# Kernel optimization log

Measured on AMD Instinct MI355X. Metric: run time of the kernel, lower is better.

Reference implementation:

```python
import jax, jax.numpy as jnp
import numpy as np

N = 4096
NFEAT = 256
NHID1 = 64
NHID2 = 32
NCLASS = 8
NHEADS = 4
NADJ = 2
ALPHA = 0.2  # leaky relu slope
NEG = -9e15


def setup_inputs() -> dict:
    key = jax.random.key(0)
    ks = jax.random.split(key, 14)
    x = jax.random.normal(ks[0], (N, NFEAT), jnp.float32)
    adj = (jax.random.uniform(ks[1], (NADJ, N, N)) < 0.01).astype(jnp.float32)
    adj = jnp.maximum(adj, jnp.eye(N, dtype=jnp.float32)[None])
    s = 0.05
    W1 = jax.random.normal(ks[2], (NADJ, NHEADS, NFEAT, NHID1), jnp.float32) * s
    a1 = jax.random.normal(ks[3], (NADJ, NHEADS, 2, NHID1), jnp.float32) * s
    W2 = jax.random.normal(ks[4], (NADJ, NHEADS, NHID1, NHID2), jnp.float32) * s
    a2 = jax.random.normal(ks[5], (NADJ, NHEADS, 2, NHID2), jnp.float32) * s
    Wi1 = jax.random.normal(ks[6], (NHID1 * NHEADS, NHID1), jnp.float32) * s
    bi1 = jnp.zeros((NHID1,), jnp.float32)
    Wi2 = jax.random.normal(ks[7], (NHID2 * NHEADS, NCLASS), jnp.float32) * s
    bi2 = jnp.zeros((NCLASS,), jnp.float32)
    Wf = jax.random.normal(ks[8], (NCLASS * NADJ, NCLASS), jnp.float32) * s
    bf = jnp.zeros((NCLASS,), jnp.float32)
    return {"x": x, "adj": adj, "W1": W1, "a1": a1, "W2": W2, "a2": a2,
            "Wi1": Wi1, "bi1": bi1, "Wi2": Wi2, "bi2": bi2, "Wf": Wf, "bf": bf}


def gat_multihead(x, adj_i, W, a):
    # x: [n, f]; adj_i: [n, n]; W: [h, f, o]; a: [h, 2, o]
    Wh = jnp.einsum('nf,hfo->hno', x, W)                 # [h, n, o]
    f_src = jnp.einsum('hno,ho->hn', Wh, a[:, 0])        # [h, n]
    f_dst = jnp.einsum('hno,ho->hn', Wh, a[:, 1])        # [h, n]
    e = jax.nn.leaky_relu(f_src[:, :, None] + f_dst[:, None, :], ALPHA)
    e = jnp.where(adj_i[None] > 0, e, NEG)               # masked scores [h, n, n]
    att = jax.nn.softmax(e, axis=-1)
    h = jnp.einsum('hnm,hmo->hno', att, Wh)              # aggregate
    h = jax.nn.elu(h)                                     # concat=True -> elu
    n = x.shape[0]
    return jnp.transpose(h, (1, 0, 2)).reshape(n, -1)     # [n, h*o]


def reference(x, adj, W1, a1, W2, a2, Wi1, bi1, Wi2, bi2, Wf, bf):
    outs = []
    for i in range(NADJ):  # small fixed loop over adjacency graphs
        xi = gat_multihead(x, adj[i], W1[i], a1[i])
        xi = jax.nn.elu(xi @ Wi1 + bi1)
        xi = gat_multihead(xi, adj[i], W2[i], a2[i])
        xi = jax.nn.elu(xi @ Wi2 + bi2)
        outs.append(xi)
    out = jnp.concatenate(outs, axis=1) @ Wf + bf         # [n, nclass]
    l1_loss = jnp.mean(jnp.abs(Wf))
    return jax.nn.log_softmax(out, axis=1), l1_loss
```

## Files before the change

### kernel.cpp

```cpp
#include <hip/hip_runtime.h>
#include <hip/hip_bf16.h>

#define NN 4096
#define NFEAT 256
#define NHID1 64
#define NHID2 32
#define NCLASS 8
#define NHEADS 4
#define NADJ 2
#define CAP 128

__device__ __forceinline__ unsigned short f2bf(float v) {
  unsigned int x = __float_as_uint(v);
  return (unsigned short)((x + 0x7fffu + ((x >> 16) & 1u)) >> 16);
}

template <int KDIM, int NDIM, int RPTY>
__device__ __forceinline__ void gemm_body(
    const float* __restrict__ A, const float* __restrict__ B,
    unsigned short* __restrict__ C, const float* __restrict__ ag,
    float* __restrict__ fsrc, float* __restrict__ fdst, const int row0b,
    float* __restrict__ sA, float* __restrict__ sB) {
  constexpr int KT = 32;
  constexpr int TX = NDIM / 4;
  constexpr int TY = 256 / TX;
  constexpr int BR = TY * RPTY;
  constexpr int LDA = BR + 4;
  constexpr int LDB = NDIM + 4;
  const int tid = threadIdx.x;
  const int tx = tid % TX, ty = tid / TX;
  const int c0 = tx * 4;
  float acc[RPTY][4];
#pragma unroll
  for (int i = 0; i < RPTY; ++i)
#pragma unroll
    for (int j = 0; j < 4; ++j) acc[i][j] = 0.f;

  for (int kt = 0; kt < KDIM; kt += KT) {
    __syncthreads();
    for (int i = tid; i < BR * (KT / 4); i += 256) {
      const int r = i / (KT / 4), e = i % (KT / 4);
      const float4 v = *(const float4*)(A + (size_t)(row0b + r) * KDIM + kt + e * 4);
      sA[(e * 4 + 0) * LDA + r] = v.x;
      sA[(e * 4 + 1) * LDA + r] = v.y;
      sA[(e * 4 + 2) * LDA + r] = v.z;
      sA[(e * 4 + 3) * LDA + r] = v.w;
    }
    for (int i = tid; i < KT * (NDIM / 4); i += 256) {
      const int k = i / (NDIM / 4), cc = i % (NDIM / 4);
      *(float4*)&sB[k * LDB + cc * 4] = *(const float4*)(B + (size_t)(kt + k) * NDIM + cc * 4);
    }
    __syncthreads();
#pragma unroll
    for (int k = 0; k < KT; ++k) {
      const float4 t = *(const float4*)&sA[k * LDA + ty * 4];
      const float a4[4] = {t.x, t.y, t.z, t.w};
      const float4 bv = *(const float4*)&sB[k * LDB + c0];
      const float b4[4] = {bv.x, bv.y, bv.z, bv.w};
#pragma unroll
      for (int i = 0; i < RPTY; ++i)
#pragma unroll
        for (int j = 0; j < 4; ++j) acc[i][j] += a4[i] * b4[j];
    }
  }
#pragma unroll
  for (int i = 0; i < RPTY; ++i) {
    const int row = row0b + ty * RPTY + i;
    ushort4 o;
    o.x = f2bf(acc[i][0]); o.y = f2bf(acc[i][1]);
    o.z = f2bf(acc[i][2]); o.w = f2bf(acc[i][3]);
    *(ushort4*)(C + (size_t)row * NDIM + c0) = o;
  }
  float aS[4], aD[4];
#pragma unroll
  for (int j = 0; j < 4; ++j) { aS[j] = ag[c0 + j]; aD[j] = ag[NDIM + c0 + j]; }
#pragma unroll
  for (int i = 0; i < RPTY; ++i) {
    float s = 0.f, d = 0.f;
#pragma unroll
    for (int j = 0; j < 4; ++j) { s += acc[i][j] * aS[j]; d += acc[i][j] * aD[j]; }
#pragma unroll
    for (int off = TX / 2; off; off >>= 1) {
      s += __shfl_xor(s, off);
      d += __shfl_xor(d, off);
    }
    if (tx == 0) {
      const int row = row0b + ty * RPTY + i;
      fsrc[row] = s;
      fdst[row] = d;
    }
  }
}

__global__ __launch_bounds__(256) void k1_gemm_edges(
    const float* __restrict__ x, const float* __restrict__ W1,
    const float* __restrict__ a1, unsigned short* __restrict__ Wh1,
    float* __restrict__ fs1, float* __restrict__ fd1,
    const float* __restrict__ adj, int* __restrict__ eidx,
    int* __restrict__ ecnt) {
  __shared__ float sA[32 * (64 + 4)];
  __shared__ float sB[32 * (64 + 4)];
  constexpr int NB_GEMM = (NN / 64) * NHEADS * NADJ;
  if (blockIdx.x < NB_GEMM) {
    int b = blockIdx.x;
    const int tile = b % (NN / 64); b /= (NN / 64);
    const int h = b % NHEADS;
    const int g = b / NHEADS;
    const int gh = g * NHEADS + h;
    gemm_body<NFEAT, NHID1, 4>(
        x, W1 + (size_t)gh * NFEAT * NHID1, Wh1 + (size_t)gh * NN * NHID1,
        a1 + (size_t)gh * 2 * NHID1, fs1 + (size_t)gh * NN,
        fd1 + (size_t)gh * NN, tile * 64, sA, sB);
  } else {
    const int wave = threadIdx.x >> 6;
    const int lane = threadIdx.x & 63;
    const int r = (blockIdx.x - NB_GEMM) * 4 + wave;
    const float4* row = (const float4*)(adj + (size_t)r * NN);
    int* out = eidx + (size_t)r * CAP;
    int base = 0;
    for (int c = 0; c < NN; c += 256) {
      const float4 v = row[(c >> 2) + lane];
      const int j0 = c + lane * 4;
      const float vt[4] = {v.x, v.y, v.z, v.w};
#pragma unroll
      for (int t = 0; t < 4; ++t) {
        const bool hit = vt[t] > 0.f;
        const unsigned long long m = __ballot(hit);
        if (hit) {
          const int pos = base + __popcll(m & ((1ull << lane) - 1ull));
          if (pos < CAP) out[pos] = j0 + t;
        }
        base += __popcll(m);
      }
    }
    if (lane == 0) ecnt[r] = base < CAP ? base : CAP;
  }
}

#define GATB(ACC, JJ, OO)                                                      \
  {                                                                            \
    const float w_ = wgt[wave][JJ];                                            \
    const uint4 v_ = *(const uint4*)(WhH + (size_t)midx[wave][JJ] * OO + c8);  \
    ACC[0] += w_ * __uint_as_float(v_.x << 16);                                \
    ACC[1] += w_ * __uint_as_float(v_.x & 0xffff0000u);                        \
    ACC[2] += w_ * __uint_as_float(v_.y << 16);                                \
    ACC[3] += w_ * __uint_as_float(v_.y & 0xffff0000u);                        \
    ACC[4] += w_ * __uint_as_float(v_.z << 16);                                \
    ACC[5] += w_ * __uint_as_float(v_.z & 0xffff0000u);                        \
    ACC[6] += w_ * __uint_as_float(v_.w << 16);                                \
    ACC[7] += w_ * __uint_as_float(v_.w & 0xffff0000u);                        \
  }

__global__ __launch_bounds__(256) void aggregate1(
    const unsigned short* __restrict__ Wh, const float* __restrict__ fsrc,
    const float* __restrict__ fdst, const int* __restrict__ eidx,
    const int* __restrict__ ecnt, float* __restrict__ Hout) {
  constexpr int O = NHID1;
  constexpr int CPL = O / 8;
  constexpr int EPW = 64 / CPL;
  __shared__ float wgt[4][CAP];
  __shared__ int midx[4][CAP];
  const int wave = threadIdx.x >> 6;
  const int lane = threadIdx.x & 63;
  const int n = blockIdx.x * 4 + wave;
  const int h = blockIdx.y, g = blockIdx.z;
  const int gh = g * NHEADS + h;
  const int cnt = ecnt[(size_t)g * NN + n];
  const int* ei = eidx + (size_t)(g * NN + n) * CAP;
  const float fs = fsrc[(size_t)gh * NN + n];
  const float* fd = fdst + (size_t)gh * NN;
  float mx = -3.4e38f;
  for (int j = lane; j < cnt; j += 64) {
    const int m = ei[j];
    float e = fs + fd[m];
    e = e > 0.f ? e : 0.2f * e;
    midx[wave][j] = m;
    wgt[wave][j] = e;
    mx = fmaxf(mx, e);
  }
  for (int off = 32; off; off >>= 1) mx = fmaxf(mx, __shfl_xor(mx, off));
  float sm = 0.f;
  for (int j = lane; j < cnt; j += 64) {
    const float w = __expf(wgt[wave][j] - mx);
    wgt[wave][j] = w;
    sm += w;
  }
  for (int off = 32; off; off >>= 1) sm += __shfl_xor(sm, off);
  const unsigned short* WhH = Wh + (size_t)gh * NN * O;
  const int sub = lane / CPL;
  const int c8 = (lane % CPL) * 8;
  float A0[8] = {0, 0, 0, 0, 0, 0, 0, 0};
  float A1[8] = {0, 0, 0, 0, 0, 0, 0, 0};
  int j = sub;
  for (; j + EPW < cnt; j += 2 * EPW) {
    GATB(A0, j, O);
    GATB(A1, j + EPW, O);
  }
  for (; j < cnt; j += EPW) GATB(A0, j, O);
#pragma unroll
  for (int q = 0; q < 8; ++q) A0[q] += A1[q];
#pragma unroll
  for (int off = CPL; off < 64; off <<= 1)
#pragma unroll
    for (int q = 0; q < 8; ++q) A0[q] += __shfl_xor(A0[q], off);
  if (lane < CPL) {
    const float inv = 1.f / sm;
    float o[8];
#pragma unroll
    for (int q = 0; q < 8; ++q) {
      o[q] = A0[q] * inv;
      o[q] = o[q] > 0.f ? o[q] : (__expf(o[q]) - 1.f);
    }
    float* dst = Hout + (size_t)g * NN * (NHEADS * O) + (size_t)n * (NHEADS * O) +
                 h * O + lane * 8;
    float4 o0, o1;
    o0.x = o[0]; o0.y = o[1]; o0.z = o[2]; o0.w = o[3];
    o1.x = o[4]; o1.y = o[5]; o1.z = o[6]; o1.w = o[7];
    *(float4*)dst = o0;
    *(float4*)(dst + 4) = o1;
  }
}

__global__ __launch_bounds__(256) void k3_inter_gemm2(
    const float* __restrict__ h1, const float* __restrict__ Wi1,
    const float* __restrict__ bi1, const float* __restrict__ W2,
    const float* __restrict__ a2, unsigned short* __restrict__ Wh2,
    float* __restrict__ fs2, float* __restrict__ fd2) {
  __shared__ float sA[32 * 36];
  __shared__ float sB[32 * 68];
  __shared__ float x1s[32 * 68];
  __shared__ float W2s[NHEADS * 64 * 32];
  const int g = blockIdx.y;
  const int n0 = blockIdx.x * 32;
  const int tid = threadIdx.x;
  const float* A = h1 + (size_t)g * NN * (NHEADS * NHID1);

  const int tx = tid & 15, ty = tid >> 4;
  const int c0 = tx * 4;
  float acc[2][4] = {{0.f, 0.f, 0.f, 0.f}, {0.f, 0.f, 0.f, 0.f}};
  for (int kt = 0; kt < 256; kt += 32) {
    __syncthreads();
    for (int i = tid; i < 32 * 8; i += 256) {
      const int r = i >> 3, e = i & 7;
      const float4 v = *(const float4*)(A + (size_t)(n0 + r) * 256 + kt + e * 4);
      sA[(e * 4 + 0) * 36 + r] = v.x;
      sA[(e * 4 + 1) * 36 + r] = v.y;
      sA[(e * 4 + 2) * 36 + r] = v.z;
      sA[(e * 4 + 3) * 36 + r] = v.w;
    }
    for (int i = tid; i < 32 * 16; i += 256) {
      const int k = i >> 4, cc = i & 15;
      *(float4*)&sB[k * 68 + cc * 4] = *(const float4*)(Wi1 + (size_t)(kt + k) * 64 + cc * 4);
    }
    __syncthreads();
#pragma unroll
    for (int k = 0; k < 32; ++k) {
      const float2 t = *(const float2*)&sA[k * 36 + ty * 2];
      const float4 bv = *(const float4*)&sB[k * 68 + c0];
      const float b4[4] = {bv.x, bv.y, bv.z, bv.w};
#pragma unroll
      for (int j = 0; j < 4; ++j) {
        acc[0][j] += t.x * b4[j];
        acc[1][j] += t.y * b4[j];
      }
    }
  }
  {
    const float4 bb = *(const float4*)&bi1[c0];
    const float b4[4] = {bb.x, bb.y, bb.z, bb.w};
#pragma unroll
    for (int i = 0; i < 2; ++i) {
      float4 o;
      float* op = (float*)&o;
#pragma unroll
      for (int j = 0; j < 4; ++j) {
        float v = acc[i][j] + b4[j];
        op[j] = v > 0.f ? v : (__expf(v) - 1.f);
      }
      *(float4*)&x1s[(ty * 2 + i) * 68 + c0] = o;
    }
  }
  {
    const float4* w2p = (const float4*)(W2 + (size_t)g * NHEADS * NHID1 * NHID2);
    for (int i = tid; i < 2048; i += 256) ((float4*)W2s)[i] = w2p[i];
  }
  __syncthreads();

  const int c = tid & 31, rg = tid >> 5;
  for (int h = 0; h < NHEADS; ++h) {
    const int gh = g * NHEADS + h;
    float a4[4] = {0.f, 0.f, 0.f, 0.f};
    for (int k = 0; k < 64; ++k) {
      const float w = W2s[(h * 64 + k) * 32 + c];
#pragma unroll
      for (int i = 0; i < 4; ++i) a4[i] += x1s[(rg * 4 + i) * 68 + k] * w;
    }
    const float* ag = a2 + (size_t)gh * 2 * NHID2;
    const float aS = ag[c], aD = ag[NHID2 + c];
#pragma unroll
    for (int i = 0; i < 4; ++i) {
      const int row = n0 + rg * 4 + i;
      Wh2[((size_t)gh * NN + row) * NHID2 + c] = f2bf(a4[i]);
      float s = a4[i] * aS, d = a4[i] * aD;
#pragma unroll
      for (int off = 16; off; off >>= 1) {
        s += __shfl_xor(s, off);
        d += __shfl_xor(d, off);
      }
      if (c == 0) {
        fs2[(size_t)gh * NN + row] = s;
        fd2[(size_t)gh * NN + row] = d;
      }
    }
  }
}

__global__ __launch_bounds__(512) void k4_agg2_tail(
    const unsigned short* __restrict__ Wh2, const float* __restrict__ fs2,
    const float* __restrict__ fd2, const int* __restrict__ eidx,
    const int* __restrict__ ecnt, const float* __restrict__ Wi2,
    const float* __restrict__ bi2, const float* __restrict__ Wf,
    const float* __restrict__ bfv, float* __restrict__ out) {
  constexpr int O = NHID2;
  __shared__ float Wi2s[128 * 8];
  __shared__ float WfS[16 * 8];
  __shared__ float h2cat[2][260];
  __shared__ float cat[2][17];
  __shared__ float wgt[8][CAP];
  __shared__ int midx[2][2][CAP];
  const int n0 = blockIdx.x * 2;
  const int tid = threadIdx.x;
  const int wave = tid >> 6;
  const int lane = tid & 63;

  for (int i = tid; i < 256; i += 512) ((float4*)Wi2s)[i] = ((const float4*)Wi2)[i];
  if (tid < 32) ((float4*)WfS)[tid] = ((const float4*)Wf)[tid];
  for (int i = tid; i < 4 * CAP; i += 512) {
    const int g_ = i >> 8, rr = (i >> 7) & 1, j = i & (CAP - 1);
    midx[g_][rr][j] = eidx[(size_t)(g_ * NN + n0 + rr) * CAP + j];
  }
  __syncthreads();

  const int g = wave >> 2, h = wave & 3;
  const int gh = g * NHEADS + h;
  const unsigned short* WhH = Wh2 + (size_t)gh * NN * O;
  const float* fdv = fd2 + (size_t)gh * NN;
  for (int rr = 0; rr < 2; ++rr) {
    const int n = n0 + rr;
    const int cnt = ecnt[g * NN + n];
    const float fsv = fs2[(size_t)gh * NN + n];
    float mx = -3.4e38f;
    for (int j = lane; j < cnt; j += 64) {
      float e = fsv + fdv[midx[g][rr][j]];
      e = e > 0.f ? e : 0.2f * e;
      wgt[wave][j] = e;
      mx = fmaxf(mx, e);
    }
    for (int off = 32; off; off >>= 1) mx = fmaxf(mx, __shfl_xor(mx, off));
    float sm = 0.f;
    for (int j = lane; j < cnt; j += 64) {
      const float w = __expf(wgt[wave][j] - mx);
      wgt[wave][j] = w;
      sm += w;
    }
    for (int off = 32; off; off >>= 1) sm += __shfl_xor(sm, off);
    const int sub = lane >> 2;
    const int c8 = (lane & 3) * 8;
    float A0[8] = {0, 0, 0, 0, 0, 0, 0, 0};
    float A1[8] = {0, 0, 0, 0, 0, 0, 0, 0};
    {
      const int wv = wave;
      const int* mi = midx[g][rr];
      int j = sub;
      for (; j + 16 < cnt; j += 32) {
        {
          const float w_ = wgt[wv][j];
          const uint4 v_ = *(const uint4*)(WhH + (size_t)mi[j] * O + c8);
          A0[0] += w_ * __uint_as_float(v_.x << 16);
          A0[1] += w_ * __uint_as_float(v_.x & 0xffff0000u);
          A0[2] += w_ * __uint_as_float(v_.y << 16);
          A0[3] += w_ * __uint_as_float(v_.y & 0xffff0000u);
          A0[4] += w_ * __uint_as_float(v_.z << 16);
          A0[5] += w_ * __uint_as_float(v_.z & 0xffff0000u);
          A0[6] += w_ * __uint_as_float(v_.w << 16);
          A0[7] += w_ * __uint_as_float(v_.w & 0xffff0000u);
        }
        {
          const float w_ = wgt[wv][j + 16];
          const uint4 v_ = *(const uint4*)(WhH + (size_t)mi[j + 16] * O + c8);
          A1[0] += w_ * __uint_as_float(v_.x << 16);
          A1[1] += w_ * __uint_as_float(v_.x & 0xffff0000u);
          A1[2] += w_ * __uint_as_float(v_.y << 16);
          A1[3] += w_ * __uint_as_float(v_.y & 0xffff0000u);
          A1[4] += w_ * __uint_as_float(v_.z << 16);
          A1[5] += w_ * __uint_as_float(v_.z & 0xffff0000u);
          A1[6] += w_ * __uint_as_float(v_.w << 16);
          A1[7] += w_ * __uint_as_float(v_.w & 0xffff0000u);
        }
      }
      for (; j < cnt; j += 16) {
        const float w_ = wgt[wv][j];
        const uint4 v_ = *(const uint4*)(WhH + (size_t)mi[j] * O + c8);
        A0[0] += w_ * __uint_as_float(v_.x << 16);
        A0[1] += w_ * __uint_as_float(v_.x & 0xffff0000u);
        A0[2] += w_ * __uint_as_float(v_.y << 16);
        A0[3] += w_ * __uint_as_float(v_.y & 0xffff0000u);
        A0[4] += w_ * __uint_as_float(v_.z << 16);
        A0[5] += w_ * __uint_as_float(v_.z & 0xffff0000u);
        A0[6] += w_ * __uint_as_float(v_.w << 16);
        A0[7] += w_ * __uint_as_float(v_.w & 0xffff0000u);
      }
    }
#pragma unroll
    for (int q = 0; q < 8; ++q) A0[q] += A1[q];
#pragma unroll
    for (int off = 4; off < 64; off <<= 1)
#pragma unroll
      for (int q = 0; q < 8; ++q) A0[q] += __shfl_xor(A0[q], off);
    if (lane < 4) {
      const float inv = 1.f / sm;
      float o[8];
#pragma unroll
      for (int q = 0; q < 8; ++q) {
        o[q] = A0[q] * inv;
        o[q] = o[q] > 0.f ? o[q] : (__expf(o[q]) - 1.f);
      }
      float4 o0, o1;
      o0.x = o[0]; o0.y = o[1]; o0.z = o[2]; o0.w = o[3];
      o1.x = o[4]; o1.y = o[5]; o1.z = o[6]; o1.w = o[7];
      float* dst = &h2cat[rr][g * 128 + h * O + (lane & 3) * 8];
      *(float4*)dst = o0;
      *(float4*)(dst + 4) = o1;
    }
  }
  __syncthreads();

  {
    const int r = tid >> 8, gg = (tid >> 7) & 1, c = (tid >> 4) & 7, kc = tid & 15;
    float s = 0.f;
#pragma unroll
    for (int k = kc * 8; k < kc * 8 + 8; ++k)
      s += h2cat[r][gg * 128 + k] * Wi2s[k * 8 + c];
#pragma unroll
    for (int off = 8; off; off >>= 1) s += __shfl_xor(s, off);
    if (kc == 0) {
      const float v = s + bi2[c];
      cat[r][gg * 8 + c] = v > 0.f ? v : (__expf(v) - 1.f);
    }
  }
  __syncthreads();

  if (tid < 16) {
    const int r = tid >> 3, c = tid & 7;
    float logit = bfv[c];
#pragma unroll
    for (int k = 0; k < 16; ++k) logit += cat[r][k] * WfS[k * 8 + c];
    float m = logit;
#pragma unroll
    for (int off = 4; off; off >>= 1) m = fmaxf(m, __shfl_xor(m, off));
    float s = __expf(logit - m);
#pragma unroll
    for (int off = 4; off; off >>= 1) s += __shfl_xor(s, off);
    out[(size_t)(n0 + r) * NCLASS + c] = logit - (logf(s) + m);
  }
  if (blockIdx.x == 0 && tid >= 64 && tid < 128) {
    const int t = tid - 64;
    float v = fabsf(Wf[t]) + fabsf(Wf[64 + t]);
    for (int off = 32; off; off >>= 1) v += __shfl_xor(v, off);
    if (t == 0) out[NN * NCLASS] = v * (1.f / (2 * NCLASS * NCLASS));
  }
}

extern "C" void kernel_launch(void* const* d_in, const int* in_sizes, int n_in,
                              void* d_out, int out_size, void* d_ws, size_t ws_size,
                              hipStream_t stream) {
  const float* x = (const float*)d_in[0];
  const float* adj = (const float*)d_in[1];
  const float* W1 = (const float*)d_in[2];
  const float* a1 = (const float*)d_in[3];
  const float* W2 = (const float*)d_in[4];
  const float* a2 = (const float*)d_in[5];
  const float* Wi1 = (const float*)d_in[6];
  const float* bi1 = (const float*)d_in[7];
  const float* Wi2 = (const float*)d_in[8];
  const float* bi2 = (const float*)d_in[9];
  const float* Wf = (const float*)d_in[10];
  const float* bfv = (const float*)d_in[11];
  float* out = (float*)d_out;

  char* ws = (char*)d_ws;
  int* eidx = (int*)ws;            ws += (size_t)NADJ * NN * CAP * 4;
  int* ecnt = (int*)ws;            ws += (size_t)NADJ * NN * 4;
  unsigned short* Wh1 = (unsigned short*)ws;
  ws += (size_t)NADJ * NHEADS * NN * NHID1 * 2;
  float* fs1 = (float*)ws;         ws += (size_t)NADJ * NHEADS * NN * 4;
  float* fd1 = (float*)ws;         ws += (size_t)NADJ * NHEADS * NN * 4;
  float* h1 = (float*)ws;          ws += (size_t)NADJ * NN * NHEADS * NHID1 * 4;
  unsigned short* Wh2 = (unsigned short*)ws;
  ws += (size_t)NADJ * NHEADS * NN * NHID2 * 2;
  float* fs2 = (float*)ws;         ws += (size_t)NADJ * NHEADS * NN * 4;
  float* fd2 = (float*)ws;         ws += (size_t)NADJ * NHEADS * NN * 4;

  k1_gemm_edges<<<512 + NADJ * NN / 4, 256, 0, stream>>>(
      x, W1, a1, Wh1, fs1, fd1, adj, eidx, ecnt);

  aggregate1<<<dim3(NN / 4, NHEADS, NADJ), 256, 0, stream>>>(
      Wh1, fs1, fd1, eidx, ecnt, h1);

  k3_inter_gemm2<<<dim3(NN / 32, NADJ), 256, 0, stream>>>(
      h1, Wi1, bi1, W2, a2, Wh2, fs2, fd2);

  k4_agg2_tail<<<NN / 2, 512, 0, stream>>>(
      Wh2, fs2, fd2, eidx, ecnt, Wi2, bi2, Wf, bfv, out);
}
```

Before: 110.6 us.

## Split fused inter-layer GEMM into two tiled GEMM launches and one-row agg2 blocks

Replaces the fused k3 kernel, which did the Wi1 projection and then a serial per-head W2 product from shared memory, with a generic templated tiled GEMM launched twice. The first launch writes x1 to a new workspace buffer; the second computes Wh2 per head in bf16 plus the attention coefficients over a grid with a head dimension. This exposes more parallelism than the old 256-block kernel, at the cost of an extra launch and a global round trip for x1. The layer-2 aggregation kernel now processes one node per block (twice as many blocks), and occupancy hints are added to the aggregation kernels.

```diff
diff --git a/kernel.cpp b/kernel.cpp
--- a/kernel.cpp
+++ b/kernel.cpp
@@ -151,7 +151,7 @@
     ACC[7] += w_ * __uint_as_float(v_.w & 0xffff0000u);                        \
   }
 
-__global__ __launch_bounds__(256) void aggregate1(
+__global__ __launch_bounds__(256, 8) void aggregate1(
     const unsigned short* __restrict__ Wh, const float* __restrict__ fsrc,
     const float* __restrict__ fdst, const int* __restrict__ eidx,
     const int* __restrict__ ecnt, float* __restrict__ Hout) {
@@ -221,101 +221,119 @@
   }
 }
 
-__global__ __launch_bounds__(256) void k3_inter_gemm2(
-    const float* __restrict__ h1, const float* __restrict__ Wi1,
-    const float* __restrict__ bi1, const float* __restrict__ W2,
-    const float* __restrict__ a2, unsigned short* __restrict__ Wh2,
-    float* __restrict__ fs2, float* __restrict__ fd2) {
-  __shared__ float sA[32 * 36];
-  __shared__ float sB[32 * 68];
-  __shared__ float x1s[32 * 68];
-  __shared__ float W2s[NHEADS * 64 * 32];
-  const int g = blockIdx.y;
-  const int n0 = blockIdx.x * 32;
+template <int KDIM, int NDIM, int RPTY, int ACT, int COEF, int OBF16>
+__global__ __launch_bounds__(256) void gemm_tile(
+    const float* __restrict__ A, const float* __restrict__ B,
+    const float* __restrict__ bias, void* __restrict__ C,
+    const float* __restrict__ av, float* __restrict__ fsrc,
+    float* __restrict__ fdst,
+    size_t asG, size_t bsH, size_t bsG, size_t csH, size_t csG) {
+  constexpr int KT = 32;
+  constexpr int TX = NDIM / 4;
+  constexpr int TY = 256 / TX;
+  constexpr int BR = TY * RPTY;
+  constexpr int LDA = BR + 4;
+  constexpr int LDB = NDIM + 4;
+  __shared__ float sA[KT * LDA];
+  __shared__ float sB[KT * LDB];
+  const int g = blockIdx.z, h = blockIdx.y;
+  const int gh = g * NHEADS + h;
+  const float* Ap = A + (size_t)g * asG;
+  const float* Bp = B + (size_t)g * bsG + (size_t)h * bsH;
+  const int row0b = (int)blockIdx.x * BR;
   const int tid = threadIdx.x;
-  const float* A = h1 + (size_t)g * NN * (NHEADS * NHID1);
-
-  const int tx = tid & 15, ty = tid >> 4;
+  const int tx = tid % TX, ty = tid / TX;
   const int c0 = tx * 4;
-  float acc[2][4] = {{0.f, 0.f, 0.f, 0.f}, {0.f, 0.f, 0.f, 0.f}};
-  for (int kt = 0; kt < 256; kt += 32) {
+  float acc[RPTY][4];
+#pragma unroll
+  for (int i = 0; i < RPTY; ++i)
+#pragma unroll
+    for (int j = 0; j < 4; ++j) acc[i][j] = 0.f;
+
+  for (int kt = 0; kt < KDIM; kt += KT) {
     __syncthreads();
-    for (int i = tid; i < 32 * 8; i += 256) {
-      const int r = i >> 3, e = i & 7;
-      const float4 v = *(const float4*)(A + (size_t)(n0 + r) * 256 + kt + e * 4);
-      sA[(e * 4 + 0) * 36 + r] = v.x;
-      sA[(e * 4 + 1) * 36 + r] = v.y;
-      sA[(e * 4 + 2) * 36 + r] = v.z;
-      sA[(e * 4 + 3) * 36 + r] = v.w;
-    }
-    for (int i = tid; i < 32 * 16; i += 256) {
-      const int k = i >> 4, cc = i & 15;
-      *(float4*)&sB[k * 68 + cc * 4] = *(const float4*)(Wi1 + (size_t)(kt + k) * 64 + cc * 4);
+    for (int i = tid; i < BR * (KT / 4); i += 256) {
+      const int r = i / (KT / 4), e = i % (KT / 4);
+      const float4 v = *(const float4*)(Ap + (size_t)(row0b + r) * KDIM + kt + e * 4);
+      sA[(e * 4 + 0) * LDA + r] = v.x;
+      sA[(e * 4 + 1) * LDA + r] = v.y;
+      sA[(e * 4 + 2) * LDA + r] = v.z;
+      sA[(e * 4 + 3) * LDA + r] = v.w;
+    }
+    for (int i = tid; i < KT * (NDIM / 4); i += 256) {
+      const int k = i / (NDIM / 4), cc = i % (NDIM / 4);
+      *(float4*)&sB[k * LDB + cc * 4] = *(const float4*)(Bp + (size_t)(kt + k) * NDIM + cc * 4);
     }
     __syncthreads();
 #pragma unroll
-    for (int k = 0; k < 32; ++k) {
-      const float2 t = *(const float2*)&sA[k * 36 + ty * 2];
-      const float4 bv = *(const float4*)&sB[k * 68 + c0];
+    for (int k = 0; k < KT; ++k) {
+      float a4[RPTY];
+      if constexpr (RPTY == 4) {
+        const float4 t = *(const float4*)&sA[k * LDA + ty * 4];
+        a4[0] = t.x; a4[1] = t.y; a4[2] = t.z; a4[3] = t.w;
+      } else {
+        const float2 t = *(const float2*)&sA[k * LDA + ty * 2];
+        a4[0] = t.x; a4[1] = t.y;
+      }
+      const float4 bv = *(const float4*)&sB[k * LDB + c0];
       const float b4[4] = {bv.x, bv.y, bv.z, bv.w};
 #pragma unroll
-      for (int j = 0; j < 4; ++j) {
-        acc[0][j] += t.x * b4[j];
-        acc[1][j] += t.y * b4[j];
-      }
-    }
-  }
-  {
-    const float4 bb = *(const float4*)&bi1[c0];
-    const float b4[4] = {bb.x, bb.y, bb.z, bb.w};
-#pragma unroll
-    for (int i = 0; i < 2; ++i) {
+      for (int i = 0; i < RPTY; ++i)
+#pragma unroll
+        for (int j = 0; j < 4; ++j) acc[i][j] += a4[i] * b4[j];
+    }
+  }
+  float b4[4] = {0.f, 0.f, 0.f, 0.f};
+  if (bias) {
+    const float4 bb = *(const float4*)&bias[c0];
+    b4[0] = bb.x; b4[1] = bb.y; b4[2] = bb.z; b4[3] = bb.w;
+  }
+#pragma unroll
+  for (int i = 0; i < RPTY; ++i) {
+    const int row = row0b + ty * RPTY + i;
+    float v[4];
+#pragma unroll
+    for (int j = 0; j < 4; ++j) {
+      v[j] = acc[i][j] + b4[j];
+      if (ACT == 1) v[j] = v[j] > 0.f ? v[j] : (__expf(v[j]) - 1.f);
+    }
+    if constexpr (OBF16) {
+      ushort4 o;
+      o.x = f2bf(v[0]); o.y = f2bf(v[1]); o.z = f2bf(v[2]); o.w = f2bf(v[3]);
+      *(ushort4*)((unsigned short*)C + (size_t)g * csG + (size_t)h * csH +
+                  (size_t)row * NDIM + c0) = o;
+    } else {
       float4 o;
-      float* op = (float*)&o;
-#pragma unroll
-      for (int j = 0; j < 4; ++j) {
-        float v = acc[i][j] + b4[j];
-        op[j] = v > 0.f ? v : (__expf(v) - 1.f);
-      }
-      *(float4*)&x1s[(ty * 2 + i) * 68 + c0] = o;
-    }
-  }
-  {
-    const float4* w2p = (const float4*)(W2 + (size_t)g * NHEADS * NHID1 * NHID2);
-    for (int i = tid; i < 2048; i += 256) ((float4*)W2s)[i] = w2p[i];
-  }
-  __syncthreads();
-
-  const int c = tid & 31, rg = tid >> 5;
-  for (int h = 0; h < NHEADS; ++h) {
-    const int gh = g * NHEADS + h;
-    float a4[4] = {0.f, 0.f, 0.f, 0.f};
-    for (int k = 0; k < 64; ++k) {
-      const float w = W2s[(h * 64 + k) * 32 + c];
-#pragma unroll
-      for (int i = 0; i < 4; ++i) a4[i] += x1s[(rg * 4 + i) * 68 + k] * w;
-    }
-    const float* ag = a2 + (size_t)gh * 2 * NHID2;
-    const float aS = ag[c], aD = ag[NHID2 + c];
-#pragma unroll
-    for (int i = 0; i < 4; ++i) {
-      const int row = n0 + rg * 4 + i;
-      Wh2[((size_t)gh * NN + row) * NHID2 + c] = f2bf(a4[i]);
-      float s = a4[i] * aS, d = a4[i] * aD;
-#pragma unroll
-      for (int off = 16; off; off >>= 1) {
+      o.x = v[0]; o.y = v[1]; o.z = v[2]; o.w = v[3];
+      *(float4*)((float*)C + (size_t)g * csG + (size_t)h * csH +
+                 (size_t)row * NDIM + c0) = o;
+    }
+  }
+  if constexpr (COEF) {
+    const float* ag = av + (size_t)gh * 2 * NDIM;
+    float aS[4], aD[4];
+#pragma unroll
+    for (int j = 0; j < 4; ++j) { aS[j] = ag[c0 + j]; aD[j] = ag[NDIM + c0 + j]; }
+#pragma unroll
+    for (int i = 0; i < RPTY; ++i) {
+      float s = 0.f, d = 0.f;
+#pragma unroll
+      for (int j = 0; j < 4; ++j) { s += acc[i][j] * aS[j]; d += acc[i][j] * aD[j]; }
+#pragma unroll
+      for (int off = TX / 2; off; off >>= 1) {
         s += __shfl_xor(s, off);
         d += __shfl_xor(d, off);
       }
-      if (c == 0) {
-        fs2[(size_t)gh * NN + row] = s;
-        fd2[(size_t)gh * NN + row] = d;
-      }
-    }
-  }
-}
-
-__global__ __launch_bounds__(512) void k4_agg2_tail(
+      if (tx == 0) {
+        const int row = row0b + ty * RPTY + i;
+        fsrc[(size_t)gh * NN + row] = s;
+        fdst[(size_t)gh * NN + row] = d;
+      }
+    }
+  }
+}
+
+__global__ __launch_bounds__(512, 8) void k4_agg2_tail(
     const unsigned short* __restrict__ Wh2, const float* __restrict__ fs2,
     const float* __restrict__ fd2, const int* __restrict__ eidx,
     const int* __restrict__ ecnt, const float* __restrict__ Wi2,
@@ -324,34 +342,32 @@
   constexpr int O = NHID2;
   __shared__ float Wi2s[128 * 8];
   __shared__ float WfS[16 * 8];
-  __shared__ float h2cat[2][260];
-  __shared__ float cat[2][17];
+  __shared__ float h2cat[260];
+  __shared__ float cat[17];
   __shared__ float wgt[8][CAP];
-  __shared__ int midx[2][2][CAP];
-  const int n0 = blockIdx.x * 2;
+  __shared__ int midx[2][CAP];
+  const int n = blockIdx.x;
   const int tid = threadIdx.x;
   const int wave = tid >> 6;
   const int lane = tid & 63;
 
   for (int i = tid; i < 256; i += 512) ((float4*)Wi2s)[i] = ((const float4*)Wi2)[i];
   if (tid < 32) ((float4*)WfS)[tid] = ((const float4*)Wf)[tid];
-  for (int i = tid; i < 4 * CAP; i += 512) {
-    const int g_ = i >> 8, rr = (i >> 7) & 1, j = i & (CAP - 1);
-    midx[g_][rr][j] = eidx[(size_t)(g_ * NN + n0 + rr) * CAP + j];
+  for (int i = tid; i < 2 * CAP; i += 512) {
+    const int g_ = i >> 7, j = i & (CAP - 1);
+    midx[g_][j] = eidx[(size_t)(g_ * NN + n) * CAP + j];
   }
   __syncthreads();
 
-  const int g = wave >> 2, h = wave & 3;
-  const int gh = g * NHEADS + h;
-  const unsigned short* WhH = Wh2 + (size_t)gh * NN * O;
-  const float* fdv = fd2 + (size_t)gh * NN;
-  for (int rr = 0; rr < 2; ++rr) {
-    const int n = n0 + rr;
+  {
+    const int g = wave >> 2, h = wave & 3;
+    const int gh = g * NHEADS + h;
     const int cnt = ecnt[g * NN + n];
     const float fsv = fs2[(size_t)gh * NN + n];
+    const float* fdv = fd2 + (size_t)gh * NN;
     float mx = -3.4e38f;
     for (int j = lane; j < cnt; j += 64) {
-      float e = fsv + fdv[midx[g][rr][j]];
+      float e = fsv + fdv[midx[g][j]];
       e = e > 0.f ? e : 0.2f * e;
       wgt[wave][j] = e;
       mx = fmaxf(mx, e);
@@ -364,42 +380,16 @@
       sm += w;
     }
     for (int off = 32; off; off >>= 1) sm += __shfl_xor(sm, off);
+    const unsigned short* WhH = Wh2 + (size_t)gh * NN * O;
+    const int* mi = midx[g];
     const int sub = lane >> 2;
     const int c8 = (lane & 3) * 8;
     float A0[8] = {0, 0, 0, 0, 0, 0, 0, 0};
     float A1[8] = {0, 0, 0, 0, 0, 0, 0, 0};
-    {
-      const int wv = wave;
-      const int* mi = midx[g][rr];
-      int j = sub;
-      for (; j + 16 < cnt; j += 32) {
-        {
-          const float w_ = wgt[wv][j];
-          const uint4 v_ = *(const uint4*)(WhH + (size_t)mi[j] * O + c8);
-          A0[0] += w_ * __uint_as_float(v_.x << 16);
-          A0[1] += w_ * __uint_as_float(v_.x & 0xffff0000u);
-          A0[2] += w_ * __uint_as_float(v_.y << 16);
-          A0[3] += w_ * __uint_as_float(v_.y & 0xffff0000u);
-          A0[4] += w_ * __uint_as_float(v_.z << 16);
-          A0[5] += w_ * __uint_as_float(v_.z & 0xffff0000u);
-          A0[6] += w_ * __uint_as_float(v_.w << 16);
-          A0[7] += w_ * __uint_as_float(v_.w & 0xffff0000u);
-        }
-        {
-          const float w_ = wgt[wv][j + 16];
-          const uint4 v_ = *(const uint4*)(WhH + (size_t)mi[j + 16] * O + c8);
-          A1[0] += w_ * __uint_as_float(v_.x << 16);
-          A1[1] += w_ * __uint_as_float(v_.x & 0xffff0000u);
-          A1[2] += w_ * __uint_as_float(v_.y << 16);
-          A1[3] += w_ * __uint_as_float(v_.y & 0xffff0000u);
-          A1[4] += w_ * __uint_as_float(v_.z << 16);
-          A1[5] += w_ * __uint_as_float(v_.z & 0xffff0000u);
-          A1[6] += w_ * __uint_as_float(v_.w << 16);
-          A1[7] += w_ * __uint_as_float(v_.w & 0xffff0000u);
-        }
-      }
-      for (; j < cnt; j += 16) {
-        const float w_ = wgt[wv][j];
+    int j = sub;
+    for (; j + 16 < cnt; j += 32) {
+      {
+        const float w_ = wgt[wave][j];
         const uint4 v_ = *(const uint4*)(WhH + (size_t)mi[j] * O + c8);
         A0[0] += w_ * __uint_as_float(v_.x << 16);
         A0[1] += w_ * __uint_as_float(v_.x & 0xffff0000u);
@@ -410,6 +400,30 @@
         A0[6] += w_ * __uint_as_float(v_.w << 16);
         A0[7] += w_ * __uint_as_float(v_.w & 0xffff0000u);
       }
+      {
+        const float w_ = wgt[wave][j + 16];
+        const uint4 v_ = *(const uint4*)(WhH + (size_t)mi[j + 16] * O + c8);
+        A1[0] += w_ * __uint_as_float(v_.x << 16);
+        A1[1] += w_ * __uint_as_float(v_.x & 0xffff0000u);
+        A1[2] += w_ * __uint_as_float(v_.y << 16);
+        A1[3] += w_ * __uint_as_float(v_.y & 0xffff0000u);
+        A1[4] += w_ * __uint_as_float(v_.z << 16);
+        A1[5] += w_ * __uint_as_float(v_.z & 0xffff0000u);
+        A1[6] += w_ * __uint_as_float(v_.w << 16);
+        A1[7] += w_ * __uint_as_float(v_.w & 0xffff0000u);
+      }
+    }
+    for (; j < cnt; j += 16) {
+      const float w_ = wgt[wave][j];
+      const uint4 v_ = *(const uint4*)(WhH + (size_t)mi[j] * O + c8);
+      A0[0] += w_ * __uint_as_float(v_.x << 16);
+      A0[1] += w_ * __uint_as_float(v_.x & 0xffff0000u);
+      A0[2] += w_ * __uint_as_float(v_.y << 16);
+      A0[3] += w_ * __uint_as_float(v_.y & 0xffff0000u);
+      A0[4] += w_ * __uint_as_float(v_.z << 16);
+      A0[5] += w_ * __uint_as_float(v_.z & 0xffff0000u);
+      A0[6] += w_ * __uint_as_float(v_.w << 16);
+      A0[7] += w_ * __uint_as_float(v_.w & 0xffff0000u);
     }
 #pragma unroll
     for (int q = 0; q < 8; ++q) A0[q] += A1[q];
@@ -428,7 +442,7 @@
       float4 o0, o1;
       o0.x = o[0]; o0.y = o[1]; o0.z = o[2]; o0.w = o[3];
       o1.x = o[4]; o1.y = o[5]; o1.z = o[6]; o1.w = o[7];
-      float* dst = &h2cat[rr][g * 128 + h * O + (lane & 3) * 8];
+      float* dst = &h2cat[g * 128 + h * O + (lane & 3) * 8];
       *(float4*)dst = o0;
       *(float4*)(dst + 4) = o1;
     }
@@ -436,32 +450,34 @@
   __syncthreads();
 
   {
-    const int r = tid >> 8, gg = (tid >> 7) & 1, c = (tid >> 4) & 7, kc = tid & 15;
+    const int gg = tid >> 8;
+    const int c = (tid >> 5) & 7;
+    const int kc = tid & 31;
     float s = 0.f;
 #pragma unroll
-    for (int k = kc * 8; k < kc * 8 + 8; ++k)
-      s += h2cat[r][gg * 128 + k] * Wi2s[k * 8 + c];
-#pragma unroll
-    for (int off = 8; off; off >>= 1) s += __shfl_xor(s, off);
+    for (int k = kc * 4; k < kc * 4 + 4; ++k)
+      s += h2cat[gg * 128 + k] * Wi2s[k * 8 + c];
+#pragma unroll
+    for (int off = 16; off; off >>= 1) s += __shfl_xor(s, off);
     if (kc == 0) {
       const float v = s + bi2[c];
-      cat[r][gg * 8 + c] = v > 0.f ? v : (__expf(v) - 1.f);
+      cat[gg * 8 + c] = v > 0.f ? v : (__expf(v) - 1.f);
     }
   }
   __syncthreads();
 
-  if (tid < 16) {
-    const int r = tid >> 3, c = tid & 7;
+  if (tid < 8) {
+    const int c = tid;
     float logit = bfv[c];
 #pragma unroll
-    for (int k = 0; k < 16; ++k) logit += cat[r][k] * WfS[k * 8 + c];
+    for (int k = 0; k < 16; ++k) logit += cat[k] * WfS[k * 8 + c];
     float m = logit;
 #pragma unroll
     for (int off = 4; off; off >>= 1) m = fmaxf(m, __shfl_xor(m, off));
     float s = __expf(logit - m);
 #pragma unroll
     for (int off = 4; off; off >>= 1) s += __shfl_xor(s, off);
-    out[(size_t)(n0 + r) * NCLASS + c] = logit - (logf(s) + m);
+    out[(size_t)n * NCLASS + c] = logit - (logf(s) + m);
   }
   if (blockIdx.x == 0 && tid >= 64 && tid < 128) {
     const int t = tid - 64;
@@ -496,6 +512,7 @@
   float* fs1 = (float*)ws;         ws += (size_t)NADJ * NHEADS * NN * 4;
   float* fd1 = (float*)ws;         ws += (size_t)NADJ * NHEADS * NN * 4;
   float* h1 = (float*)ws;          ws += (size_t)NADJ * NN * NHEADS * NHID1 * 4;
+  float* x1 = (float*)ws;          ws += (size_t)NADJ * NN * NHID1 * 4;
   unsigned short* Wh2 = (unsigned short*)ws;
   ws += (size_t)NADJ * NHEADS * NN * NHID2 * 2;
   float* fs2 = (float*)ws;         ws += (size_t)NADJ * NHEADS * NN * 4;
@@ -507,9 +524,15 @@
   aggregate1<<<dim3(NN / 4, NHEADS, NADJ), 256, 0, stream>>>(
       Wh1, fs1, fd1, eidx, ecnt, h1);
 
-  k3_inter_gemm2<<<dim3(NN / 32, NADJ), 256, 0, stream>>>(
-      h1, Wi1, bi1, W2, a2, Wh2, fs2, fd2);
-
-  k4_agg2_tail<<<NN / 2, 512, 0, stream>>>(
+  gemm_tile<NHEADS * NHID1, NHID1, 2, 1, 0, 0><<<dim3(NN / 32, 1, NADJ), 256, 0, stream>>>(
+      h1, Wi1, bi1, x1, nullptr, nullptr, nullptr,
+      (size_t)NN * NHEADS * NHID1, 0, 0, 0, (size_t)NN * NHID1);
+
+  gemm_tile<NHID1, NHID2, 4, 0, 1, 1><<<dim3(NN / 128, NHEADS, NADJ), 256, 0, stream>>>(
+      x1, W2, nullptr, Wh2, a2, fs2, fd2,
+      (size_t)NN * NHID1, (size_t)NHID1 * NHID2, (size_t)NHEADS * NHID1 * NHID2,
+      (size_t)NN * NHID2, (size_t)NHEADS * NN * NHID2);
+
+  k4_agg2_tail<<<NN, 512, 0, stream>>>(
       Wh2, fs2, fd2, eidx, ecnt, Wi2, bi2, Wf, bfv, out);
 }
```

Result: slower. 117.9 us (+6.6%).
